# Optimization experiments

Measured on AMD Instinct MI355X. Metric: run time of the kernel, lower is better.

The kernel has to match this reference:

```python
import jax, jax.numpy as jnp
import numpy as np

EMBED = 768
HEADS = 12
HEAD_DIM = EMBED // HEADS
HIDDEN = 3072
EPS = 1e-5


def setup_inputs() -> dict:
    key = jax.random.key(0)
    ks = jax.random.split(key, 8)
    s = lambda d: 1.0 / np.sqrt(d)
    return {
        "x": jax.random.normal(ks[0], (1, 4096, EMBED), jnp.float32),
        "ln1_w": jnp.ones((EMBED,), jnp.float32),
        "ln1_b": jnp.zeros((EMBED,), jnp.float32),
        "qkv_w": jax.random.normal(ks[1], (3 * EMBED, EMBED), jnp.float32) * s(EMBED),
        "qkv_b": jnp.zeros((3 * EMBED,), jnp.float32),
        "out_w": jax.random.normal(ks[2], (EMBED, EMBED), jnp.float32) * s(EMBED),
        "out_b": jnp.zeros((EMBED,), jnp.float32),
        "ln2_w": jnp.ones((EMBED,), jnp.float32),
        "ln2_b": jnp.zeros((EMBED,), jnp.float32),
        "fc1_w": jax.random.normal(ks[3], (HIDDEN, EMBED), jnp.float32) * s(EMBED),
        "fc1_b": jnp.zeros((HIDDEN,), jnp.float32),
        "fc2_w": jax.random.normal(ks[4], (EMBED, HIDDEN), jnp.float32) * s(HIDDEN),
        "fc2_b": jnp.zeros((EMBED,), jnp.float32),
    }


def _layernorm(x, w, b):
    mu = jnp.mean(x, axis=-1, keepdims=True)
    var = jnp.mean(jnp.square(x - mu), axis=-1, keepdims=True)
    return (x - mu) * jax.lax.rsqrt(var + EPS) * w + b


def reference(x, ln1_w, ln1_b, qkv_w, qkv_b, out_w, out_b,
              ln2_w, ln2_b, fc1_w, fc1_b, fc2_w, fc2_b):
    B, N, _ = x.shape
    # attention branch
    h = _layernorm(x, ln1_w, ln1_b)
    qkv = h @ qkv_w.T + qkv_b                      # [B,N,3E]
    qkv = qkv.reshape(B, N, 3, HEADS, HEAD_DIM)
    q = jnp.transpose(qkv[:, :, 0], (0, 2, 1, 3))  # [B,H,N,D]
    k = jnp.transpose(qkv[:, :, 1], (0, 2, 1, 3))
    v = jnp.transpose(qkv[:, :, 2], (0, 2, 1, 3))
    scores = jnp.einsum("bhqd,bhkd->bhqk", q, k) / np.sqrt(HEAD_DIM)
    probs = jax.nn.softmax(scores, axis=-1)
    attn = jnp.einsum("bhqk,bhkd->bhqd", probs, v)
    attn = jnp.transpose(attn, (0, 2, 1, 3)).reshape(B, N, EMBED)
    x = x + (attn @ out_w.T + out_b)
    # mlp branch
    h = _layernorm(x, ln2_w, ln2_b)
    h = jax.nn.gelu(h @ fc1_w.T + fc1_b, approximate=False)
    x = x + (h @ fc2_w.T + fc2_b)
    return x
```

## Files before the change

### kernel.cpp

```cpp
#include <hip/hip_runtime.h>
#include <hip/hip_bf16.h>

#define SEQ  4096
#define EMB  768
#define NH   12
#define HD   64
#define HID  3072
#define QKVC 2304

typedef __attribute__((ext_vector_type(8))) short bf16x8;
typedef __attribute__((ext_vector_type(4))) float f32x4;

#define MFMA16(a,b,c) __builtin_amdgcn_mfma_f32_16x16x32_bf16(a,b,c,0,0,0)

#define QSCL 0.18033688f
#define MFIX 16.0f

__device__ __forceinline__ unsigned short f2bf(float f){
  union { float f; unsigned u; } c; c.f = f;
  unsigned r = c.u + 0x7FFFu + ((c.u >> 16) & 1u);
  return (unsigned short)(r >> 16);
}

__device__ __forceinline__ float bf2f(unsigned short u){
  union { unsigned u; float f; } c; c.u = (unsigned)u << 16; return c.f;
}

__device__ __forceinline__ unsigned cvtpk(float a, float b){
  unsigned r;
  asm("v_cvt_pk_bf16_f32 %0, %1, %2" : "=v"(r) : "v"(a), "v"(b));
  return r;
}

__device__ __forceinline__ float gelu_f(float x){
  float x2 = x * x;
  float u  = __builtin_amdgcn_exp2f(x * fmaf(x2, 0.1029433f, 2.3022082f));
  return x * u * __builtin_amdgcn_rcpf(1.f + u);
}

__device__ __forceinline__ void gload_lds16(const unsigned short* g, unsigned short* l){
  __builtin_amdgcn_global_load_lds(
      (const __attribute__((address_space(1))) unsigned int*)g,
      (__attribute__((address_space(3))) unsigned int*)l, 16, 0, 0);
}

__global__ __launch_bounds__(256) void pre_kernel(
    const float* __restrict__ x, const float* __restrict__ w, const float* __restrict__ b,
    unsigned short* __restrict__ out,
    const float* __restrict__ s0, unsigned short* __restrict__ d0, int n0,
    const float* __restrict__ s1, unsigned short* __restrict__ d1, int n1,
    const float* __restrict__ s2, unsigned short* __restrict__ d2, int n2,
    const float* __restrict__ s3, unsigned short* __restrict__ d3, int n3)
{
  const int t = threadIdx.x;
  if (blockIdx.x < SEQ){
    const int row = blockIdx.x;
    const float* xr = x + (size_t)row * EMB;
    float v0 = xr[t], v1 = xr[t + 256], v2 = xr[t + 512];
    float s  = v0 + v1 + v2;
    float s2 = v0*v0 + v1*v1 + v2*v2;
    #pragma unroll
    for (int off = 32; off; off >>= 1){ s += __shfl_down(s, off); s2 += __shfl_down(s2, off); }
    __shared__ float rs[4], rq[4], st[2];
    int wv = t >> 6;
    if ((t & 63) == 0){ rs[wv] = s; rq[wv] = s2; }
    __syncthreads();
    if (t == 0){
      float S  = rs[0] + rs[1] + rs[2] + rs[3];
      float S2 = rq[0] + rq[1] + rq[2] + rq[3];
      float mu  = S * (1.f / 768.f);
      float var = S2 * (1.f / 768.f) - mu * mu;
      st[0] = mu; st[1] = rsqrtf(var + 1e-5f);
    }
    __syncthreads();
    float mu = st[0], rstd = st[1];
    unsigned short* orow = out + (size_t)row * EMB;
    orow[t]       = f2bf((v0 - mu) * rstd * w[t]       + b[t]);
    orow[t + 256] = f2bf((v1 - mu) * rstd * w[t + 256] + b[t + 256]);
    orow[t + 512] = f2bf((v2 - mu) * rstd * w[t + 512] + b[t + 512]);
  } else {
    long e = ((long)(blockIdx.x - SEQ) * 256 + t) << 2;
    const float* s; unsigned short* d;
    if (e < n0){ s = s0; d = d0; }
    else if ((e -= n0) < n1){ s = s1; d = d1; }
    else if ((e -= n1) < n2){ s = s2; d = d2; }
    else if ((e -= n2) < n3){ s = s3; d = d3; }
    else return;
    float4 v = *(const float4*)(s + e);
    ushort4 u;
    u.x = f2bf(v.x); u.y = f2bf(v.y); u.z = f2bf(v.z); u.w = f2bf(v.w);
    *(ushort4*)(d + e) = u;
  }
}

__global__ __launch_bounds__(256) void ln_kernel(const float* __restrict__ x,
    const float* __restrict__ w, const float* __restrict__ b,
    unsigned short* __restrict__ out)
{
  const int row = blockIdx.x;
  const float* xr = x + (size_t)row * EMB;
  const int t = threadIdx.x;
  float v0 = xr[t], v1 = xr[t + 256], v2 = xr[t + 512];
  float s  = v0 + v1 + v2;
  float s2 = v0*v0 + v1*v1 + v2*v2;
  #pragma unroll
  for (int off = 32; off; off >>= 1){ s += __shfl_down(s, off); s2 += __shfl_down(s2, off); }
  __shared__ float rs[4], rq[4], st[2];
  int wv = t >> 6;
  if ((t & 63) == 0){ rs[wv] = s; rq[wv] = s2; }
  __syncthreads();
  if (t == 0){
    float S  = rs[0] + rs[1] + rs[2] + rs[3];
    float S2 = rq[0] + rq[1] + rq[2] + rq[3];
    float mu  = S * (1.f / 768.f);
    float var = S2 * (1.f / 768.f) - mu * mu;
    st[0] = mu; st[1] = rsqrtf(var + 1e-5f);
  }
  __syncthreads();
  float mu = st[0], rstd = st[1];
  unsigned short* orow = out + (size_t)row * EMB;
  orow[t]       = f2bf((v0 - mu) * rstd * w[t]       + b[t]);
  orow[t + 256] = f2bf((v1 - mu) * rstd * w[t + 256] + b[t + 256]);
  orow[t + 512] = f2bf((v2 - mu) * rstd * w[t + 512] + b[t + 512]);
}

template<int EPI, int BM, int BN, int BK>
__global__ __launch_bounds__(256, (BM == 64 ? 4 : 3)) void gemm_kernel(
    const unsigned short* __restrict__ A, const unsigned short* __restrict__ B,
    const float* __restrict__ bias, const float* __restrict__ res,
    unsigned short* __restrict__ Ob, float* __restrict__ Of,
    int M, int N, int K)
{
  constexpr int MF  = BM / 32;
  constexpr int NF  = BN / 32;
  constexpr int KS  = BK / 32;
  constexpr int CPR = BK / 8;
  constexpr int AIT = BM * BK / 2048;
  constexpr int BIT = BN * BK / 2048;
  constexpr bool CNT = (BM == 128);
  constexpr int NBUF = CNT ? 3 : 2;
  __shared__ unsigned short sA[NBUF][BM * BK];
  __shared__ unsigned short sB[NBUF][BN * BK];
  const int tid  = threadIdx.x;
  const int w    = tid >> 6, lane = tid & 63;
  const int wr   = w >> 1,   wc   = w & 1;
  const int l15  = lane & 15, l4  = lane >> 4;
  const int nb  = gridDim.x;
  const int lin = blockIdx.x;
  const int v   = (lin & 7) * (nb >> 3) + (lin >> 3);
  const int gN  = N / BN;
  const int tm  = v / gN, tn = v % gN;
  const unsigned short* Ab = A + (size_t)tm * BM * K;
  const unsigned short* Bb = B + (size_t)tn * BN * K;

  f32x4 acc[MF][NF];
  #pragma unroll
  for (int m = 0; m < MF; ++m)
    #pragma unroll
    for (int n = 0; n < NF; ++n){ acc[m][n][0]=0.f; acc[m][n][1]=0.f; acc[m][n][2]=0.f; acc[m][n][3]=0.f; }

  #define GSTAGE(buf, kt) { \
    const int k0_ = (kt) * BK; \
    _Pragma("unroll") \
    for (int i = 0; i < AIT; ++i){ \
      int c = i * 256 + tid; int row = c / CPR; int skc = (c % CPR) ^ (row & (CPR - 1)); \
      gload_lds16(Ab + (size_t)row * K + k0_ + skc * 8, &sA[buf][(i * 256 + w * 64) * 8]); } \
    _Pragma("unroll") \
    for (int i = 0; i < BIT; ++i){ \
      int c = i * 256 + tid; int row = c / CPR; int skc = (c % CPR) ^ (row & (CPR - 1)); \
      gload_lds16(Bb + (size_t)row * K + k0_ + skc * 8, &sB[buf][(i * 256 + w * 64) * 8]); }}

  #define GCOMPUTE(buf) { \
    _Pragma("unroll") \
    for (int ks = 0; ks < KS; ++ks){ \
      bf16x8 af[MF], bg[NF]; \
      _Pragma("unroll") \
      for (int m = 0; m < MF; ++m){ \
        int row = wr * (BM / 2) + m * 16 + l15; \
        int kc  = ks * 4 + l4; \
        af[m] = *(const bf16x8*)&sA[buf][row * BK + ((kc ^ (row & (CPR - 1))) << 3)]; } \
      _Pragma("unroll") \
      for (int n = 0; n < NF; ++n){ \
        int row = wc * (BN / 2) + n * 16 + l15; \
        int kc  = ks * 4 + l4; \
        bg[n] = *(const bf16x8*)&sB[buf][row * BK + ((kc ^ (row & (CPR - 1))) << 3)]; } \
      _Pragma("unroll") \
      for (int m = 0; m < MF; ++m) \
        _Pragma("unroll") \
        for (int n = 0; n < NF; ++n) \
          acc[m][n] = MFMA16(af[m], bg[n], acc[m][n]); }}

  const int nk = K / BK;
  if (CNT){
    GSTAGE(0, 0);
    GSTAGE(1, 1);
    for (int kt = 0; kt < nk; ++kt){
      if (kt + 2 < nk) asm volatile("s_waitcnt vmcnt(4)" ::: "memory");
      else             asm volatile("s_waitcnt vmcnt(0)" ::: "memory");
      __builtin_amdgcn_s_barrier();
      if (kt + 2 < nk) GSTAGE((kt + 2) % 3, kt + 2);
      GCOMPUTE(kt % 3);
    }
  } else {
    GSTAGE(0, 0);
    int cur = 0;
    for (int kt = 0; kt < nk; ++kt){
      __syncthreads();
      if (kt + 1 < nk) GSTAGE(cur ^ 1, kt + 1);
      GCOMPUTE(cur);
      cur ^= 1;
    }
  }
  #undef GSTAGE
  #undef GCOMPUTE

  #pragma unroll
  for (int m = 0; m < MF; ++m){
    int row0 = tm * BM + wr * (BM / 2) + m * 16 + l4 * 4;
    #pragma unroll
    for (int n = 0; n < NF; ++n){
      int col = tn * BN + wc * (BN / 2) + n * 16 + l15;
      float bv = bias[col];
      #pragma unroll
      for (int r = 0; r < 4; ++r){
        int row = row0 + r;
        float v2 = acc[m][n][r] + bv;
        if (EPI == 0){
          Ob[(size_t)row * N + col] = f2bf(v2);
        } else if (EPI == 1){
          Ob[(size_t)row * N + col] = f2bf(gelu_f(v2));
        } else if (EPI == 3){
          if (col < EMB) v2 *= QSCL;
          Ob[(size_t)row * N + col] = f2bf(v2);
        } else {
          v2 += res[(size_t)row * N + col];
          Of[(size_t)row * N + col] = v2;
        }
      }
    }
  }
}

__global__ __launch_bounds__(256, 3) void attn_kernel(
    const unsigned short* __restrict__ qkv,
    unsigned short* __restrict__ pO, float* __restrict__ pl)
{
  __shared__ unsigned short sK[2][64 * 64];
  __shared__ unsigned short sVt[2][64 * 64];
  __shared__ unsigned short sEp[4][16 * 72];
  const int tid = threadIdx.x, w = tid >> 6, lane = tid & 63;
  const int l15 = lane & 15, l4 = lane >> 4;

  const int bid  = blockIdx.x;
  const int v_id = (bid & 7) * 96 + (bid >> 3);
  const int head = v_id >> 6;
  const int r6   = v_id & 63;
  const int qt   = r6 >> 1;
  const int sk   = r6 & 1;

  const int koff = EMB + head * HD;
  const int voff = 2 * EMB + head * HD;
  const int qbase = qt * 128 + w * 32;
  const int tbase = sk * 32;

  bf16x8 qf[2][2];
  #pragma unroll
  for (int qg = 0; qg < 2; ++qg){
    const unsigned short* qp = qkv + (size_t)(qbase + qg * 16 + l15) * QKVC + head * HD + l4 * 8;
    qf[qg][0] = *(const bf16x8*)qp;
    qf[qg][1] = *(const bf16x8*)(qp + 32);
  }

  f32x4 oaccT[4][2];
  #pragma unroll
  for (int i = 0; i < 4; ++i)
    #pragma unroll
    for (int qg = 0; qg < 2; ++qg){ oaccT[i][qg][0]=0.f; oaccT[i][qg][1]=0.f; oaccT[i][qg][2]=0.f; oaccT[i][qg][3]=0.f; }
  float l0 = 0.f, l1 = 0.f;

  const int krow = tid >> 3;
  const int kskc = (tid & 7) ^ (krow & 7);
  const int vp_  = tid >> 3;
  const int d0   = (tid & 7) * 8;
  const int w16  = vp_ & 15;
  const int qpos = (w16 & 1) | (((w16 >> 3) & 1) << 1) | (((w16 >> 1) & 3) << 2);
  const int Pc   = ((vp_ >> 4) << 2) | (qpos >> 2);
  const int Ps   = qpos & 3;

  #define KSTAGE(buf, t) { \
    const int kv0_ = (t) << 6; \
    gload_lds16(qkv + (size_t)(kv0_ + krow) * QKVC + koff + kskc * 8,      &sK[buf][(w * 64) * 8]); \
    gload_lds16(qkv + (size_t)(kv0_ + 32 + krow) * QKVC + koff + kskc * 8, &sK[buf][(256 + w * 64) * 8]); }

  #define VLOAD(t) { \
    const unsigned short* vp = qkv + (size_t)(((t) << 6) + vp_ * 2) * QKVC + voff + d0; \
    va = *(const bf16x8*)vp; \
    vb = *(const bf16x8*)(vp + QKVC); }

  #define VCOMMIT(buf) { \
    _Pragma("unroll") \
    for (int i = 0; i < 8; ++i){ \
      unsigned pk = (unsigned)(unsigned short)va[i] | ((unsigned)(unsigned short)vb[i] << 16); \
      *(unsigned*)&sVt[buf][(d0 + i) * 64 + ((Pc ^ (tid & 7) ^ i) << 3) + Ps * 2] = pk; \
    } }

  bf16x8 va, vb;
  KSTAGE(0, tbase);
  VLOAD(tbase);
  VCOMMIT(0);

  for (int tt = 0; tt < 32; ++tt){
    const int cur = tt & 1;
    __syncthreads();
    const bool pre = (tt < 31);
    if (pre){
      KSTAGE(cur ^ 1, tbase + tt + 1);
      VLOAD(tbase + tt + 1);
    }

    f32x4 sf[4][2];
    #pragma unroll
    for (int i = 0; i < 4; ++i)
      #pragma unroll
      for (int qg = 0; qg < 2; ++qg){ sf[i][qg][0]=0.f; sf[i][qg][1]=0.f; sf[i][qg][2]=0.f; sf[i][qg][3]=0.f; }
    __builtin_amdgcn_s_setprio(1);
    #pragma unroll
    for (int ks = 0; ks < 2; ++ks){
      bf16x8 kf[4];
      #pragma unroll
      for (int nb = 0; nb < 4; ++nb){
        int row = 16 * nb + l15;
        kf[nb] = *(const bf16x8*)&sK[cur][(row * 8 + ((4 * ks + l4) ^ (row & 7))) * 8];
      }
      #pragma unroll
      for (int nb = 0; nb < 4; ++nb){
        sf[nb][0] = MFMA16(kf[nb], qf[0][ks], sf[nb][0]);
        sf[nb][1] = MFMA16(kf[nb], qf[1][ks], sf[nb][1]);
      }
    }
    __builtin_amdgcn_s_setprio(0);

    unsigned pbw[2][2][4];
    {
      float ps0 = 0.f, ps1 = 0.f;
      #pragma unroll
      for (int nb = 0; nb < 4; ++nb){
        float p0[4], p1[4];
        #pragma unroll
        for (int r = 0; r < 4; ++r){
          p0[r] = __builtin_amdgcn_exp2f(sf[nb][0][r] - MFIX); ps0 += p0[r];
          p1[r] = __builtin_amdgcn_exp2f(sf[nb][1][r] - MFIX); ps1 += p1[r];
        }
        pbw[0][nb >> 1][(nb & 1) * 2]     = cvtpk(p0[0], p0[1]);
        pbw[0][nb >> 1][(nb & 1) * 2 + 1] = cvtpk(p0[2], p0[3]);
        pbw[1][nb >> 1][(nb & 1) * 2]     = cvtpk(p1[0], p1[1]);
        pbw[1][nb >> 1][(nb & 1) * 2 + 1] = cvtpk(p1[2], p1[3]);
      }
      ps0 += __shfl_xor(ps0, 16); ps0 += __shfl_xor(ps0, 32);
      ps1 += __shfl_xor(ps1, 16); ps1 += __shfl_xor(ps1, 32);
      l0 += ps0; l1 += ps1;
    }

    __builtin_amdgcn_s_setprio(1);
    {
      bf16x8 vv[2][4];
      #pragma unroll
      for (int ks = 0; ks < 2; ++ks)
        #pragma unroll
        for (int db = 0; db < 4; ++db){
          int d = 16 * db + l15;
          int cp = (4 * ks + l4) ^ ((d >> 3) & 7) ^ (d & 7);
          vv[ks][db] = *(const bf16x8*)&sVt[cur][d * 64 + cp * 8];
        }
      union { unsigned uw[4]; bf16x8 v; } pb;
      #pragma unroll
      for (int qg = 0; qg < 2; ++qg){
        bf16x8 pb0, pb1;
        pb.uw[0]=pbw[qg][0][0]; pb.uw[1]=pbw[qg][0][1]; pb.uw[2]=pbw[qg][0][2]; pb.uw[3]=pbw[qg][0][3]; pb0 = pb.v;
        pb.uw[0]=pbw[qg][1][0]; pb.uw[1]=pbw[qg][1][1]; pb.uw[2]=pbw[qg][1][2]; pb.uw[3]=pbw[qg][1][3]; pb1 = pb.v;
        #pragma unroll
        for (int db = 0; db < 4; ++db){
          oaccT[db][qg] = MFMA16(vv[0][db], pb0, oaccT[db][qg]);
          oaccT[db][qg] = MFMA16(vv[1][db], pb1, oaccT[db][qg]);
        }
      }
    }
    __builtin_amdgcn_s_setprio(0);

    if (pre) VCOMMIT(cur ^ 1);
  }

  #pragma unroll
  for (int qg = 0; qg < 2; ++qg){
    unsigned short* sPw = sEp[w];
    #pragma unroll
    for (int db = 0; db < 4; ++db)
      #pragma unroll
      for (int dw = 0; dw < 2; ++dw){
        unsigned pk = cvtpk(oaccT[db][qg][2 * dw], oaccT[db][qg][2 * dw + 1]);
        *(unsigned*)&sPw[l15 * 72 + 16 * db + 4 * l4 + 2 * dw] = pk;
      }
    int qe = lane >> 2, de = (lane & 3) * 16;
    bf16x8 r0 = *(const bf16x8*)&sPw[qe * 72 + de];
    bf16x8 r1 = *(const bf16x8*)&sPw[qe * 72 + de + 8];
    unsigned short* op = pO + ((size_t)(sk * NH + head) * SEQ + qbase + qg * 16 + qe) * 64 + de;
    *(bf16x8*)op = r0;
    *(bf16x8*)(op + 8) = r1;
  }
  if (lane < 16){
    size_t r = (size_t)(sk * NH + head) * SEQ + qbase + l15;
    pl[r]      = l0;
    pl[r + 16] = l1;
  }
  #undef KSTAGE
  #undef VLOAD
  #undef VCOMMIT
}

__global__ __launch_bounds__(256) void comb_kernel(
    const unsigned short* __restrict__ pO, const float* __restrict__ pl,
    unsigned short* __restrict__ o)
{
  const int t = threadIdx.x;
  const int row = blockIdx.x * 64 + (t >> 2);
  const int dseg = (t & 3) * 16;
  float inv = 1.f / (pl[row] + pl[NH * SEQ + row]);
  const unsigned short* p0 = pO + (size_t)row * 64 + dseg;
  const unsigned short* p1 = p0 + (size_t)NH * SEQ * 64;
  bf16x8 x0 = *(const bf16x8*)p0, x1 = *(const bf16x8*)(p0 + 8);
  bf16x8 y0 = *(const bf16x8*)p1, y1 = *(const bf16x8*)(p1 + 8);
  const int head = row >> 12, q = row & (SEQ - 1);
  unsigned short* op = o + (size_t)q * EMB + head * HD + dseg;
  union { unsigned uw[4]; bf16x8 v; } r0, r1;
  #pragma unroll
  for (int i = 0; i < 4; ++i){
    r0.uw[i] = cvtpk(inv * (bf2f((unsigned short)x0[2*i])   + bf2f((unsigned short)y0[2*i])),
                     inv * (bf2f((unsigned short)x0[2*i+1]) + bf2f((unsigned short)y0[2*i+1])));
    r1.uw[i] = cvtpk(inv * (bf2f((unsigned short)x1[2*i])   + bf2f((unsigned short)y1[2*i])),
                     inv * (bf2f((unsigned short)x1[2*i+1]) + bf2f((unsigned short)y1[2*i+1])));
  }
  *(bf16x8*)op = r0.v;
  *(bf16x8*)(op + 8) = r1.v;
}

extern "C" void kernel_launch(void* const* d_in, const int* in_sizes, int n_in,
                              void* d_out, int out_size, void* d_ws, size_t ws_size,
                              hipStream_t stream)
{
  const float* x    = (const float*)d_in[0];
  const float* ln1w = (const float*)d_in[1];
  const float* ln1b = (const float*)d_in[2];
  const float* qkvw = (const float*)d_in[3];
  const float* qkvb = (const float*)d_in[4];
  const float* outw = (const float*)d_in[5];
  const float* outb = (const float*)d_in[6];
  const float* ln2w = (const float*)d_in[7];
  const float* ln2b = (const float*)d_in[8];
  const float* fc1w = (const float*)d_in[9];
  const float* fc1b = (const float*)d_in[10];
  const float* fc2w = (const float*)d_in[11];
  const float* fc2b = (const float*)d_in[12];
  float* out = (float*)d_out;

  char* ws = (char*)d_ws;
  unsigned short* wqkv = (unsigned short*)ws; ws += (size_t)QKVC * EMB * 2;
  unsigned short* wout = (unsigned short*)ws; ws += (size_t)EMB * EMB * 2;
  unsigned short* wfc1 = (unsigned short*)ws; ws += (size_t)HID * EMB * 2;
  unsigned short* wfc2 = (unsigned short*)ws; ws += (size_t)EMB * HID * 2;
  unsigned short* h1   = (unsigned short*)ws; ws += (size_t)SEQ * EMB * 2;
  unsigned short* qkv  = (unsigned short*)ws; ws += (size_t)SEQ * QKVC * 2;
  unsigned short* h3   = (unsigned short*)ws; ws += (size_t)SEQ * HID * 2;
  unsigned short* attnb = h1;
  unsigned short* h2    = qkv;
  unsigned short* pO  = h3;
  float*          pl  = (float*)(h3 + (size_t)2 * NH * SEQ * 64);

  const int n0 = QKVC * EMB, n1 = EMB * EMB, n2 = HID * EMB, n3 = EMB * HID;
  pre_kernel<<<SEQ + (n0 + n1 + n2 + n3) / 4 / 256, 256, 0, stream>>>(
      x, ln1w, ln1b, h1,
      qkvw, wqkv, n0, outw, wout, n1, fc1w, wfc1, n2, fc2w, wfc2, n3);

  gemm_kernel<3, 128, 128, 32><<<(SEQ / 128) * (QKVC / 128), 256, 0, stream>>>(
      h1, wqkv, qkvb, nullptr, qkv, nullptr, SEQ, QKVC, EMB);

  attn_kernel<<<SEQ / 128 * NH * 2, 256, 0, stream>>>(qkv, pO, pl);
  comb_kernel<<<NH * SEQ / 64, 256, 0, stream>>>(pO, pl, attnb);

  gemm_kernel<2, 64, 64, 64><<<(SEQ / 64) * (EMB / 64), 256, 0, stream>>>(
      attnb, wout, outb, x, nullptr, out, SEQ, EMB, EMB);

  ln_kernel<<<SEQ, 256, 0, stream>>>(out, ln2w, ln2b, h2);

  gemm_kernel<1, 128, 128, 32><<<(SEQ / 128) * (HID / 128), 256, 0, stream>>>(
      h2, wfc1, fc1b, nullptr, h3, nullptr, SEQ, HID, EMB);

  gemm_kernel<2, 64, 64, 64><<<(SEQ / 64) * (EMB / 64), 256, 0, stream>>>(
      h3, wfc2, fc2b, out, nullptr, out, SEQ, EMB, HID);
}
```

Before: 197.5 us.

## Widen attention query tile to 256 and split KV four ways

Each attention block now covers 256 queries (64 per wave) and a quarter of the keys, so every K/V tile staged in LDS is reused by twice as many queries. The score/exp/PV loop is restructured into two 32-key halves to keep register pressure bounded despite four query groups per wave. The combine kernel now merges four partial outputs, and the partial row sums are stored in the output buffer, which is still free at that point. The costs are more accumulator registers per wave, which may lower occupancy, and more partial-output traffic in the combine step.

```diff
diff --git a/kernel.cpp b/kernel.cpp
--- a/kernel.cpp
+++ b/kernel.cpp
@@ -255,28 +255,28 @@
   const int v_id = (bid & 7) * 96 + (bid >> 3);
   const int head = v_id >> 6;
   const int r6   = v_id & 63;
-  const int qt   = r6 >> 1;
-  const int sk   = r6 & 1;
+  const int qt   = r6 >> 2;
+  const int sk   = r6 & 3;
 
   const int koff = EMB + head * HD;
   const int voff = 2 * EMB + head * HD;
-  const int qbase = qt * 128 + w * 32;
-  const int tbase = sk * 32;
-
-  bf16x8 qf[2][2];
-  #pragma unroll
-  for (int qg = 0; qg < 2; ++qg){
+  const int qbase = qt * 256 + w * 64;
+  const int tbase = sk * 16;
+
+  bf16x8 qf[4][2];
+  #pragma unroll
+  for (int qg = 0; qg < 4; ++qg){
     const unsigned short* qp = qkv + (size_t)(qbase + qg * 16 + l15) * QKVC + head * HD + l4 * 8;
     qf[qg][0] = *(const bf16x8*)qp;
     qf[qg][1] = *(const bf16x8*)(qp + 32);
   }
 
-  f32x4 oaccT[4][2];
+  f32x4 oaccT[4][4];
   #pragma unroll
   for (int i = 0; i < 4; ++i)
     #pragma unroll
-    for (int qg = 0; qg < 2; ++qg){ oaccT[i][qg][0]=0.f; oaccT[i][qg][1]=0.f; oaccT[i][qg][2]=0.f; oaccT[i][qg][3]=0.f; }
-  float l0 = 0.f, l1 = 0.f;
+    for (int qg = 0; qg < 4; ++qg){ oaccT[i][qg][0]=0.f; oaccT[i][qg][1]=0.f; oaccT[i][qg][2]=0.f; oaccT[i][qg][3]=0.f; }
+  float lsum[4] = {0.f, 0.f, 0.f, 0.f};
 
   const int krow = tid >> 3;
   const int kskc = (tid & 7) ^ (krow & 7);
@@ -309,89 +309,68 @@
   VLOAD(tbase);
   VCOMMIT(0);
 
-  for (int tt = 0; tt < 32; ++tt){
+  for (int tt = 0; tt < 16; ++tt){
     const int cur = tt & 1;
     __syncthreads();
-    const bool pre = (tt < 31);
+    const bool pre = (tt < 15);
     if (pre){
       KSTAGE(cur ^ 1, tbase + tt + 1);
       VLOAD(tbase + tt + 1);
     }
 
-    f32x4 sf[4][2];
-    #pragma unroll
-    for (int i = 0; i < 4; ++i)
+    #pragma unroll
+    for (int h = 0; h < 2; ++h){
+      unsigned pbw[4][4];
       #pragma unroll
-      for (int qg = 0; qg < 2; ++qg){ sf[i][qg][0]=0.f; sf[i][qg][1]=0.f; sf[i][qg][2]=0.f; sf[i][qg][3]=0.f; }
-    __builtin_amdgcn_s_setprio(1);
-    #pragma unroll
-    for (int ks = 0; ks < 2; ++ks){
-      bf16x8 kf[4];
-      #pragma unroll
-      for (int nb = 0; nb < 4; ++nb){
-        int row = 16 * nb + l15;
-        kf[nb] = *(const bf16x8*)&sK[cur][(row * 8 + ((4 * ks + l4) ^ (row & 7))) * 8];
-      }
-      #pragma unroll
-      for (int nb = 0; nb < 4; ++nb){
-        sf[nb][0] = MFMA16(kf[nb], qf[0][ks], sf[nb][0]);
-        sf[nb][1] = MFMA16(kf[nb], qf[1][ks], sf[nb][1]);
-      }
-    }
-    __builtin_amdgcn_s_setprio(0);
-
-    unsigned pbw[2][2][4];
-    {
-      float ps0 = 0.f, ps1 = 0.f;
-      #pragma unroll
-      for (int nb = 0; nb < 4; ++nb){
-        float p0[4], p1[4];
+      for (int nbl = 0; nbl < 2; ++nbl){
+        const int row = 16 * (2 * h + nbl) + l15;
+        bf16x8 kf0 = *(const bf16x8*)&sK[cur][(row * 8 + ( l4      ^ (row & 7))) * 8];
+        bf16x8 kf1 = *(const bf16x8*)&sK[cur][(row * 8 + ((4 + l4) ^ (row & 7))) * 8];
+        __builtin_amdgcn_s_setprio(1);
+        f32x4 s0, s1, s2, s3;
+        s0[0]=0.f;s0[1]=0.f;s0[2]=0.f;s0[3]=0.f; s1=s0; s2=s0; s3=s0;
+        s0 = MFMA16(kf0, qf[0][0], s0); s1 = MFMA16(kf0, qf[1][0], s1);
+        s2 = MFMA16(kf0, qf[2][0], s2); s3 = MFMA16(kf0, qf[3][0], s3);
+        s0 = MFMA16(kf1, qf[0][1], s0); s1 = MFMA16(kf1, qf[1][1], s1);
+        s2 = MFMA16(kf1, qf[2][1], s2); s3 = MFMA16(kf1, qf[3][1], s3);
+        __builtin_amdgcn_s_setprio(0);
+        f32x4 sv[4] = {s0, s1, s2, s3};
         #pragma unroll
-        for (int r = 0; r < 4; ++r){
-          p0[r] = __builtin_amdgcn_exp2f(sf[nb][0][r] - MFIX); ps0 += p0[r];
-          p1[r] = __builtin_amdgcn_exp2f(sf[nb][1][r] - MFIX); ps1 += p1[r];
-        }
-        pbw[0][nb >> 1][(nb & 1) * 2]     = cvtpk(p0[0], p0[1]);
-        pbw[0][nb >> 1][(nb & 1) * 2 + 1] = cvtpk(p0[2], p0[3]);
-        pbw[1][nb >> 1][(nb & 1) * 2]     = cvtpk(p1[0], p1[1]);
-        pbw[1][nb >> 1][(nb & 1) * 2 + 1] = cvtpk(p1[2], p1[3]);
-      }
-      ps0 += __shfl_xor(ps0, 16); ps0 += __shfl_xor(ps0, 32);
-      ps1 += __shfl_xor(ps1, 16); ps1 += __shfl_xor(ps1, 32);
-      l0 += ps0; l1 += ps1;
-    }
-
-    __builtin_amdgcn_s_setprio(1);
-    {
-      bf16x8 vv[2][4];
-      #pragma unroll
-      for (int ks = 0; ks < 2; ++ks)
-        #pragma unroll
-        for (int db = 0; db < 4; ++db){
-          int d = 16 * db + l15;
-          int cp = (4 * ks + l4) ^ ((d >> 3) & 7) ^ (d & 7);
-          vv[ks][db] = *(const bf16x8*)&sVt[cur][d * 64 + cp * 8];
-        }
-      union { unsigned uw[4]; bf16x8 v; } pb;
-      #pragma unroll
-      for (int qg = 0; qg < 2; ++qg){
-        bf16x8 pb0, pb1;
-        pb.uw[0]=pbw[qg][0][0]; pb.uw[1]=pbw[qg][0][1]; pb.uw[2]=pbw[qg][0][2]; pb.uw[3]=pbw[qg][0][3]; pb0 = pb.v;
-        pb.uw[0]=pbw[qg][1][0]; pb.uw[1]=pbw[qg][1][1]; pb.uw[2]=pbw[qg][1][2]; pb.uw[3]=pbw[qg][1][3]; pb1 = pb.v;
-        #pragma unroll
-        for (int db = 0; db < 4; ++db){
-          oaccT[db][qg] = MFMA16(vv[0][db], pb0, oaccT[db][qg]);
-          oaccT[db][qg] = MFMA16(vv[1][db], pb1, oaccT[db][qg]);
+        for (int qg = 0; qg < 4; ++qg){
+          float p0 = __builtin_amdgcn_exp2f(sv[qg][0] - MFIX);
+          float p1 = __builtin_amdgcn_exp2f(sv[qg][1] - MFIX);
+          float p2 = __builtin_amdgcn_exp2f(sv[qg][2] - MFIX);
+          float p3 = __builtin_amdgcn_exp2f(sv[qg][3] - MFIX);
+          lsum[qg] += (p0 + p1) + (p2 + p3);
+          pbw[qg][nbl * 2]     = cvtpk(p0, p1);
+          pbw[qg][nbl * 2 + 1] = cvtpk(p2, p3);
         }
       }
-    }
-    __builtin_amdgcn_s_setprio(0);
+      bf16x8 vv[4];
+      #pragma unroll
+      for (int db = 0; db < 4; ++db){
+        int d = 16 * db + l15;
+        int cp = (4 * h + l4) ^ ((d >> 3) & 7) ^ (d & 7);
+        vv[db] = *(const bf16x8*)&sVt[cur][d * 64 + cp * 8];
+      }
+      union { unsigned uw[4]; bf16x8 v; } pb;
+      __builtin_amdgcn_s_setprio(1);
+      #pragma unroll
+      for (int qg = 0; qg < 4; ++qg){
+        pb.uw[0]=pbw[qg][0]; pb.uw[1]=pbw[qg][1]; pb.uw[2]=pbw[qg][2]; pb.uw[3]=pbw[qg][3];
+        bf16x8 pv = pb.v;
+        #pragma unroll
+        for (int db = 0; db < 4; ++db)
+          oaccT[db][qg] = MFMA16(vv[db], pv, oaccT[db][qg]);
+      }
+      __builtin_amdgcn_s_setprio(0);
+    }
 
     if (pre) VCOMMIT(cur ^ 1);
   }
 
   #pragma unroll
-  for (int qg = 0; qg < 2; ++qg){
+  for (int qg = 0; qg < 4; ++qg){
     unsigned short* sPw = sEp[w];
     #pragma unroll
     for (int db = 0; db < 4; ++db)
@@ -407,10 +386,13 @@
     *(bf16x8*)op = r0;
     *(bf16x8*)(op + 8) = r1;
   }
-  if (lane < 16){
-    size_t r = (size_t)(sk * NH + head) * SEQ + qbase + l15;
-    pl[r]      = l0;
-    pl[r + 16] = l1;
+  #pragma unroll
+  for (int qg = 0; qg < 4; ++qg){
+    float l = lsum[qg];
+    l += __shfl_xor(l, 16);
+    l += __shfl_xor(l, 32);
+    if (lane < 16)
+      pl[(size_t)(sk * NH + head) * SEQ + qbase + qg * 16 + l15] = l;
   }
   #undef KSTAGE
   #undef VLOAD
@@ -424,20 +406,28 @@
   const int t = threadIdx.x;
   const int row = blockIdx.x * 64 + (t >> 2);
   const int dseg = (t & 3) * 16;
-  float inv = 1.f / (pl[row] + pl[NH * SEQ + row]);
-  const unsigned short* p0 = pO + (size_t)row * 64 + dseg;
-  const unsigned short* p1 = p0 + (size_t)NH * SEQ * 64;
-  bf16x8 x0 = *(const bf16x8*)p0, x1 = *(const bf16x8*)(p0 + 8);
-  bf16x8 y0 = *(const bf16x8*)p1, y1 = *(const bf16x8*)(p1 + 8);
+  const size_t S = (size_t)NH * SEQ;
+  float inv = 1.f / (((pl[row] + pl[S + row]) + (pl[2 * S + row] + pl[3 * S + row])));
+  const unsigned short* p = pO + (size_t)row * 64 + dseg;
+  bf16x8 a0 = *(const bf16x8*)p,                 a1 = *(const bf16x8*)(p + 8);
+  bf16x8 b0 = *(const bf16x8*)(p + S * 64),      b1 = *(const bf16x8*)(p + S * 64 + 8);
+  bf16x8 c0 = *(const bf16x8*)(p + 2 * S * 64),  c1 = *(const bf16x8*)(p + 2 * S * 64 + 8);
+  bf16x8 e0 = *(const bf16x8*)(p + 3 * S * 64),  e1 = *(const bf16x8*)(p + 3 * S * 64 + 8);
   const int head = row >> 12, q = row & (SEQ - 1);
   unsigned short* op = o + (size_t)q * EMB + head * HD + dseg;
   union { unsigned uw[4]; bf16x8 v; } r0, r1;
   #pragma unroll
   for (int i = 0; i < 4; ++i){
-    r0.uw[i] = cvtpk(inv * (bf2f((unsigned short)x0[2*i])   + bf2f((unsigned short)y0[2*i])),
-                     inv * (bf2f((unsigned short)x0[2*i+1]) + bf2f((unsigned short)y0[2*i+1])));
-    r1.uw[i] = cvtpk(inv * (bf2f((unsigned short)x1[2*i])   + bf2f((unsigned short)y1[2*i])),
-                     inv * (bf2f((unsigned short)x1[2*i+1]) + bf2f((unsigned short)y1[2*i+1])));
+    float x0 = (bf2f((unsigned short)a0[2*i])   + bf2f((unsigned short)b0[2*i]))
+             + (bf2f((unsigned short)c0[2*i])   + bf2f((unsigned short)e0[2*i]));
+    float x1 = (bf2f((unsigned short)a0[2*i+1]) + bf2f((unsigned short)b0[2*i+1]))
+             + (bf2f((unsigned short)c0[2*i+1]) + bf2f((unsigned short)e0[2*i+1]));
+    float y0 = (bf2f((unsigned short)a1[2*i])   + bf2f((unsigned short)b1[2*i]))
+             + (bf2f((unsigned short)c1[2*i])   + bf2f((unsigned short)e1[2*i]));
+    float y1 = (bf2f((unsigned short)a1[2*i+1]) + bf2f((unsigned short)b1[2*i+1]))
+             + (bf2f((unsigned short)c1[2*i+1]) + bf2f((unsigned short)e1[2*i+1]));
+    r0.uw[i] = cvtpk(inv * x0, inv * x1);
+    r1.uw[i] = cvtpk(inv * y0, inv * y1);
   }
   *(bf16x8*)op = r0.v;
   *(bf16x8*)(op + 8) = r1.v;
@@ -473,7 +463,7 @@
   unsigned short* attnb = h1;
   unsigned short* h2    = qkv;
   unsigned short* pO  = h3;
-  float*          pl  = (float*)(h3 + (size_t)2 * NH * SEQ * 64);
+  float*          pl  = out;
 
   const int n0 = QKVC * EMB, n1 = EMB * EMB, n2 = HID * EMB, n3 = EMB * HID;
   pre_kernel<<<SEQ + (n0 + n1 + n2 + n3) / 4 / 256, 256, 0, stream>>>(
@@ -483,7 +473,7 @@
   gemm_kernel<3, 128, 128, 32><<<(SEQ / 128) * (QKVC / 128), 256, 0, stream>>>(
       h1, wqkv, qkvb, nullptr, qkv, nullptr, SEQ, QKVC, EMB);
 
-  attn_kernel<<<SEQ / 128 * NH * 2, 256, 0, stream>>>(qkv, pO, pl);
+  attn_kernel<<<SEQ / 256 * NH * 4, 256, 0, stream>>>(qkv, pO, pl);
   comb_kernel<<<NH * SEQ / 64, 256, 0, stream>>>(pO, pl, attnb);
 
   gemm_kernel<2, 64, 64, 64><<<(SEQ / 64) * (EMB / 64), 256, 0, stream>>>(
```

New measurement: 202.7 us. 2.7% more time.
